# Optimization experiments

Hardware: AMD Instinct MI355X
Metric: run time of the kernel (lower is better)

The kernel has to match this reference:

```python
import jax, jax.numpy as jnp
import numpy as np

D_MODEL = 1024
NUM_HEADS = 16
D_K = D_MODEL // NUM_HEADS
B, S = 4, 2048
NEG = -1e20


def setup_inputs() -> dict:
    key = jax.random.key(0)
    ks = jax.random.split(key, 12)
    def lin(kw, kb):
        # torch nn.Linear init: U(-1/sqrt(in), 1/sqrt(in)), weight shape [out, in]
        bound = 1.0 / np.sqrt(D_MODEL)
        W = jax.random.uniform(kw, (D_MODEL, D_MODEL), jnp.float32, -bound, bound)
        b = jax.random.uniform(kb, (D_MODEL,), jnp.float32, -bound, bound)
        return W, b
    Wq, bq = lin(ks[0], ks[1])
    Wk, bk = lin(ks[2], ks[3])
    Wv, bv = lin(ks[4], ks[5])
    Wo, bo = lin(ks[6], ks[7])
    q = jax.random.normal(ks[8], (B, S, D_MODEL), jnp.float32)
    k = jax.random.normal(ks[9], (B, S, D_MODEL), jnp.float32)
    v = jax.random.normal(ks[10], (B, S, D_MODEL), jnp.float32)
    # causal mask, broadcastable [1,1,S,S]; mask==0 positions are masked out
    mask = jnp.tril(jnp.ones((S, S), jnp.int32))[None, None]
    return {"q": q, "k": k, "v": v, "mask": mask,
            "Wq": Wq, "bq": bq, "Wk": Wk, "bk": bk,
            "Wv": Wv, "bv": bv, "Wo": Wo, "bo": bo}


def _split_heads(x):
    b, s, _ = x.shape
    return x.reshape(b, s, NUM_HEADS, D_K).transpose(0, 2, 1, 3)  # [b,h,s,dk]


def reference(q, k, v, mask, Wq, bq, Wk, bk, Wv, bv, Wo, bo):
    qh = _split_heads(q @ Wq.T + bq)
    kh = _split_heads(k @ Wk.T + bk)
    vh = _split_heads(v @ Wv.T + bv)
    scores = jnp.einsum('bhqd,bhkd->bhqk', qh, kh) / jnp.sqrt(jnp.float32(D_K))
    scores = jnp.where(mask == 0, jnp.float32(NEG), scores)
    attn = jax.nn.softmax(scores, axis=-1)  # dropout is identity in eval mode
    out = jnp.einsum('bhqk,bhkd->bhqd', attn, vh)
    out = out.transpose(0, 2, 1, 3).reshape(q.shape[0], -1, D_MODEL)
    return out @ Wo.T + bo, attn
```

## Files before the change

### kernel.cpp

```cpp
#include <hip/hip_runtime.h>
#include <stdint.h>

#define S_LEN 2048
#define NHEADS 16
#define DK 64
#define DMODEL 1024
#define PS_STRIDE 72
#define S_MASK -3.0e4f

typedef __bf16 bf16;
typedef __bf16 bf16x8 __attribute__((ext_vector_type(8)));
typedef float f32x4 __attribute__((ext_vector_type(4)));
typedef uint32_t u32;

#define MFMA(a, b, c) __builtin_amdgcn_mfma_f32_16x16x32_bf16((a), (b), (c), 0, 0, 0)

__device__ __forceinline__ bf16x8 cvt8(f32x4 a, f32x4 b) {
  bf16x8 w;
  w[0] = (bf16)a[0]; w[1] = (bf16)a[1]; w[2] = (bf16)a[2]; w[3] = (bf16)a[3];
  w[4] = (bf16)b[0]; w[5] = (bf16)b[1]; w[6] = (bf16)b[2]; w[7] = (bf16)b[3];
  return w;
}

__device__ __forceinline__ void async16(const void* g, void* lds_uniform) {
  __builtin_amdgcn_global_load_lds((const __attribute__((address_space(1))) u32*)g,
                                   (__attribute__((address_space(3))) u32*)lds_uniform,
                                   16, 0, 0);
}

__device__ __forceinline__ void stage_tile(const bf16* gbase, size_t rstride,
                                           bf16* buf, int wave, int lane) {
#pragma unroll
  for (int i = 0; i < 2; ++i) {
    int c = i * 256 + wave * 64 + lane;
    int r = c >> 3, ch = c & 7;
    int chg = ch ^ (r & 7);
    const bf16* src = gbase + (size_t)r * rstride + chg * 8;
    char* dst = (char*)buf + (size_t)(i * 256 + wave * 64) * 16;
    async16(src, dst);
  }
}

__global__ __launch_bounds__(256) void cvt_f32_bf16(const float* __restrict__ src,
                                                    bf16* __restrict__ dst, int n8) {
  int stride = gridDim.x * blockDim.x;
  for (int i = blockIdx.x * blockDim.x + threadIdx.x; i < n8; i += stride) {
    f32x4 a = ((const f32x4*)src)[2 * i];
    f32x4 b = ((const f32x4*)src)[2 * i + 1];
    ((bf16x8*)dst)[i] = cvt8(a, b);
  }
}

template <int MODE, typename OutT>
__global__ __launch_bounds__(256, 2) void gemm_bias(const bf16* __restrict__ X,
                                                    const bf16* __restrict__ W,
                                                    const float* __restrict__ bias,
                                                    OutT* __restrict__ out) {
  __shared__ __attribute__((aligned(16))) bf16 At[128 * 32];
  __shared__ __attribute__((aligned(16))) bf16 Bt[128 * 32];
  const int tid = threadIdx.x;
  const int wave = tid >> 6;
  const int lane = tid & 63;
  const int col16 = lane & 15;
  const int kg = lane >> 4;
  const int m0 = blockIdx.x * 128;
  const int n0 = blockIdx.y * 128;
  const int wm = (wave >> 1) * 64;
  const int wn = (wave & 1) * 64;

  f32x4 acc[4][4] = {};

  for (int k0 = 0; k0 < 1024; k0 += 32) {
    __syncthreads();
#pragma unroll
    for (int is = 0; is < 2; ++is) {
      int idx = wave * 64 + is * 256 + lane;
      int row = idx >> 2, ch = idx & 3;
      const char* ga = (const char*)(X + (size_t)(m0 + row) * 1024 + k0) + ch * 16;
      const char* gb = (const char*)(W + (size_t)(n0 + row) * 1024 + k0) + ch * 16;
      async16(ga, (char*)At + (size_t)(wave * 64 + is * 256) * 16);
      async16(gb, (char*)Bt + (size_t)(wave * 64 + is * 256) * 16);
    }
    __syncthreads();

    bf16x8 af[4], bfr[4];
#pragma unroll
    for (int i = 0; i < 4; ++i)
      af[i] = *(const bf16x8*)&At[(wm + i * 16 + col16) * 32 + kg * 8];
#pragma unroll
    for (int j = 0; j < 4; ++j)
      bfr[j] = *(const bf16x8*)&Bt[(wn + j * 16 + col16) * 32 + kg * 8];
#pragma unroll
    for (int i = 0; i < 4; ++i)
#pragma unroll
      for (int j = 0; j < 4; ++j) acc[i][j] = MFMA(af[i], bfr[j], acc[i][j]);
  }

#pragma unroll
  for (int j = 0; j < 4; ++j) {
    int n = n0 + wn + j * 16 + col16;
    float bj = bias[n];
#pragma unroll
    for (int i = 0; i < 4; ++i) {
#pragma unroll
      for (int r = 0; r < 4; ++r) {
        int m = m0 + wm + i * 16 + kg * 4 + r;
        float v = acc[i][j][r] + bj;
        size_t o;
        if (MODE == 0) {
          o = (size_t)m * 1024 + n;
        } else {
          int b = m >> 11, s = m & 2047;
          int h = n >> 6, d = n & 63;
          if (MODE == 1)
            o = ((size_t)(b * 16 + h) * 2048 + s) * 64 + d;
          else
            o = ((size_t)(b * 16 + h) * 64 + d) * 2048 + s;
        }
        out[o] = (OutT)v;
      }
    }
  }
}

__global__ __launch_bounds__(256, 2) void attn_fused(const bf16* __restrict__ Qh,
                                                     const bf16* __restrict__ Kh,
                                                     const bf16* __restrict__ Vt,
                                                     float* __restrict__ attn,
                                                     bf16* __restrict__ O) {
  __shared__ __attribute__((aligned(16))) bf16 Klds[2][64 * 64];
  __shared__ __attribute__((aligned(16))) bf16 Vlds[2][64 * 64];
  __shared__ __attribute__((aligned(16))) bf16 Ps[128 * PS_STRIDE];
  const int tid = threadIdx.x;
  const int wave = tid >> 6;
  const int lane = tid & 63;
  const int col16 = lane & 15;
  const int kg = lane >> 4;
  const int pr = blockIdx.x;
  const int bh = blockIdx.z * NHEADS + blockIdx.y;

  const bf16* qb = Qh + (size_t)bh * S_LEN * DK;
  const bf16* kb = Kh + (size_t)bh * S_LEN * DK;
  const bf16* vb = Vt + (size_t)bh * DK * S_LEN;
  float* ab = attn + (size_t)bh * S_LEN * S_LEN;
  const int b_ = bh >> 4, h_ = bh & 15;

#pragma unroll 1
  for (int sp = 0; sp < 2; ++sp) {
    const int bq = sp ? (15 - pr) : pr;
    const int q0 = bq * 128;
    const int jt_max = 2 * bq + 1;

    bf16x8 qf[2][2];
#pragma unroll
    for (int fr = 0; fr < 2; ++fr)
#pragma unroll
      for (int kk = 0; kk < 2; ++kk) {
        bf16x8 v = *(const bf16x8*)&qb[(size_t)(q0 + wave * 32 + fr * 16 + col16) * DK +
                                       kk * 32 + kg * 8];
        bf16x8 sc;
#pragma unroll
        for (int e = 0; e < 8; ++e) sc[e] = (bf16)((float)v[e] * 0.125f);
        qf[fr][kk] = sc;
      }

    float l_run[2][4] = {};

    stage_tile(kb, DK, Klds[0], wave, lane);
    __syncthreads();
    int cur = 0;
    for (int jt = 0; jt <= jt_max; ++jt) {
      if (jt < jt_max) stage_tile(kb + (size_t)(jt + 1) * 64 * DK, DK, Klds[cur ^ 1], wave, lane);
      const int j0 = jt * 64;
      f32x4 s[2][4] = {};
#pragma unroll
      for (int kk = 0; kk < 2; ++kk) {
        bf16x8 kf[4];
#pragma unroll
        for (int fc = 0; fc < 4; ++fc) {
          int rr = fc * 16 + col16;
          kf[fc] = *(const bf16x8*)&Klds[cur][rr * 64 + (((kk << 2) + kg) ^ (rr & 7)) * 8];
        }
#pragma unroll
        for (int fr = 0; fr < 2; ++fr)
#pragma unroll
          for (int fc = 0; fc < 4; ++fc) s[fr][fc] = MFMA(qf[fr][kk], kf[fc], s[fr][fc]);
      }
      if (jt >= 2 * bq) {
#pragma unroll
        for (int fr = 0; fr < 2; ++fr)
#pragma unroll
          for (int fc = 0; fc < 4; ++fc)
#pragma unroll
            for (int r = 0; r < 4; ++r) {
              int qi = q0 + wave * 32 + fr * 16 + kg * 4 + r;
              int j = j0 + fc * 16 + col16;
              if (j > qi) s[fr][fc][r] = S_MASK;
            }
      }
#pragma unroll
      for (int fr = 0; fr < 2; ++fr)
#pragma unroll
        for (int r = 0; r < 4; ++r)
          l_run[fr][r] += (__expf(s[fr][0][r]) + __expf(s[fr][1][r])) +
                          (__expf(s[fr][2][r]) + __expf(s[fr][3][r]));
      __syncthreads();
      cur ^= 1;
    }
    float linv[2][4];
#pragma unroll
    for (int fr = 0; fr < 2; ++fr)
#pragma unroll
      for (int r = 0; r < 4; ++r) {
        float l = l_run[fr][r];
#pragma unroll
        for (int dd = 1; dd < 16; dd <<= 1) l += __shfl_xor(l, dd, 64);
        linv[fr][r] = 1.f / l;
      }

    f32x4 o[2][4] = {};
    stage_tile(kb, DK, Klds[0], wave, lane);
    stage_tile(vb, S_LEN, Vlds[0], wave, lane);
    __syncthreads();
    cur = 0;
    for (int jt = 0; jt <= jt_max; ++jt) {
      if (jt < jt_max) {
        stage_tile(kb + (size_t)(jt + 1) * 64 * DK, DK, Klds[cur ^ 1], wave, lane);
        stage_tile(vb + (jt + 1) * 64, S_LEN, Vlds[cur ^ 1], wave, lane);
      }
      const int j0 = jt * 64;
      f32x4 s[2][4] = {};
#pragma unroll
      for (int kk = 0; kk < 2; ++kk) {
        bf16x8 kf[4];
#pragma unroll
        for (int fc = 0; fc < 4; ++fc) {
          int rr = fc * 16 + col16;
          kf[fc] = *(const bf16x8*)&Klds[cur][rr * 64 + (((kk << 2) + kg) ^ (rr & 7)) * 8];
        }
#pragma unroll
        for (int fr = 0; fr < 2; ++fr)
#pragma unroll
          for (int fc = 0; fc < 4; ++fc) s[fr][fc] = MFMA(qf[fr][kk], kf[fc], s[fr][fc]);
      }
      if (jt >= 2 * bq) {
#pragma unroll
        for (int fr = 0; fr < 2; ++fr)
#pragma unroll
          for (int fc = 0; fc < 4; ++fc)
#pragma unroll
            for (int r = 0; r < 4; ++r) {
              int qi = q0 + wave * 32 + fr * 16 + kg * 4 + r;
              int j = j0 + fc * 16 + col16;
              if (j > qi) s[fr][fc][r] = S_MASK;
            }
      }
#pragma unroll
      for (int fr = 0; fr < 2; ++fr)
#pragma unroll
        for (int fc = 0; fc < 4; ++fc)
#pragma unroll
          for (int r = 0; r < 4; ++r) {
            float p = __expf(s[fr][fc][r]) * linv[fr][r];
            int row = wave * 32 + fr * 16 + kg * 4 + r;
            int col = fc * 16 + col16;
            ab[(size_t)(q0 + row) * S_LEN + j0 + col] = p;
            Ps[row * PS_STRIDE + col] = (bf16)p;
          }
      __syncthreads();
#pragma unroll
      for (int kk = 0; kk < 2; ++kk) {
        bf16x8 pf[2], vf[4];
#pragma unroll
        for (int fr = 0; fr < 2; ++fr)
          pf[fr] = *(const bf16x8*)&Ps[(wave * 32 + fr * 16 + col16) * PS_STRIDE + kk * 32 + kg * 8];
#pragma unroll
        for (int fc = 0; fc < 4; ++fc) {
          int rr = fc * 16 + col16;
          vf[fc] = *(const bf16x8*)&Vlds[cur][rr * 64 + (((kk << 2) + kg) ^ (rr & 7)) * 8];
        }
#pragma unroll
        for (int fr = 0; fr < 2; ++fr)
#pragma unroll
          for (int fc = 0; fc < 4; ++fc) o[fr][fc] = MFMA(pf[fr], vf[fc], o[fr][fc]);
      }
      __syncthreads();
      cur ^= 1;
    }

    {
      f32x4 z = {0.f, 0.f, 0.f, 0.f};
      for (int jt = jt_max + 1; jt < S_LEN / 64; ++jt) {
        const int j0 = jt * 64;
#pragma unroll
        for (int rep = 0; rep < 8; ++rep) {
          int idx = rep * 256 + tid;
          int row = idx >> 4, c = idx & 15;
          *(f32x4*)&ab[(size_t)(q0 + row) * S_LEN + j0 + c * 4] = z;
        }
      }
    }

#pragma unroll
    for (int fr = 0; fr < 2; ++fr)
#pragma unroll
      for (int fc = 0; fc < 4; ++fc)
#pragma unroll
        for (int r = 0; r < 4; ++r) {
          size_t row = (size_t)b_ * S_LEN + q0 + wave * 32 + fr * 16 + kg * 4 + r;
          O[row * DMODEL + h_ * 64 + fc * 16 + col16] = (bf16)o[fr][fc][r];
        }
  }
}

static inline void cvt_launch(const float* src, bf16* dst, size_t n, hipStream_t stream) {
  int n8 = (int)(n / 8);
  int blocks = (n8 + 255) / 256;
  if (blocks > 2048) blocks = 2048;
  cvt_f32_bf16<<<blocks, 256, 0, stream>>>(src, dst, n8);
}

extern "C" void kernel_launch(void* const* d_in, const int* in_sizes, int n_in,
                              void* d_out, int out_size, void* d_ws, size_t ws_size,
                              hipStream_t stream) {
  (void)in_sizes; (void)n_in; (void)out_size; (void)ws_size;
  const float* q = (const float*)d_in[0];
  const float* k = (const float*)d_in[1];
  const float* v = (const float*)d_in[2];
  const float* Wq = (const float*)d_in[4];
  const float* bq = (const float*)d_in[5];
  const float* Wk = (const float*)d_in[6];
  const float* bk = (const float*)d_in[7];
  const float* Wv = (const float*)d_in[8];
  const float* bv = (const float*)d_in[9];
  const float* Wo = (const float*)d_in[10];
  const float* bo = (const float*)d_in[11];

  float* out = (float*)d_out;
  float* attn = out + (size_t)8192 * 1024;

  const size_t NX = (size_t)8192 * 1024;
  const size_t NW = (size_t)1024 * 1024;
  bf16* Qh = (bf16*)d_ws;
  bf16* Kh = Qh + NX;
  bf16* Vt = Kh + NX;
  bf16* O = Vt + NX;
  bf16* Xbf = O + NX;
  bf16* Wbf = Xbf + NX;

  dim3 gg(64, 8), bb(256);

  cvt_launch(q, Xbf, NX, stream);
  cvt_launch(Wq, Wbf, NW, stream);
  gemm_bias<1, bf16><<<gg, bb, 0, stream>>>(Xbf, Wbf, bq, Qh);

  cvt_launch(k, Xbf, NX, stream);
  cvt_launch(Wk, Wbf, NW, stream);
  gemm_bias<1, bf16><<<gg, bb, 0, stream>>>(Xbf, Wbf, bk, Kh);

  cvt_launch(v, Xbf, NX, stream);
  cvt_launch(Wv, Wbf, NW, stream);
  gemm_bias<2, bf16><<<gg, bb, 0, stream>>>(Xbf, Wbf, bv, Vt);

  attn_fused<<<dim3(8, NHEADS, 4), bb, 0, stream>>>(Qh, Kh, Vt, attn, O);

  cvt_launch(Wo, Wbf, NW, stream);
  gemm_bias<0, float><<<gg, bb, 0, stream>>>(O, Wbf, bo, out);
}
```

Baseline: 529.4 us.

## Use eight waves per attention block with one 16-row fragment each

```diff
diff --git a/kernel.cpp b/kernel.cpp
--- a/kernel.cpp
+++ b/kernel.cpp
@@ -28,17 +28,14 @@
                                    16, 0, 0);
 }
 
-__device__ __forceinline__ void stage_tile(const bf16* gbase, size_t rstride,
-                                           bf16* buf, int wave, int lane) {
-#pragma unroll
-  for (int i = 0; i < 2; ++i) {
-    int c = i * 256 + wave * 64 + lane;
-    int r = c >> 3, ch = c & 7;
-    int chg = ch ^ (r & 7);
-    const bf16* src = gbase + (size_t)r * rstride + chg * 8;
-    char* dst = (char*)buf + (size_t)(i * 256 + wave * 64) * 16;
-    async16(src, dst);
-  }
+__device__ __forceinline__ void stage_tile8(const bf16* gbase, size_t rstride,
+                                            bf16* buf, int wave, int lane) {
+  int c = wave * 64 + lane;
+  int r = c >> 3, ch = c & 7;
+  int chg = ch ^ (r & 7);
+  const bf16* src = gbase + (size_t)r * rstride + chg * 8;
+  char* dst = (char*)buf + (size_t)(wave * 64) * 16;
+  async16(src, dst);
 }
 
 __global__ __launch_bounds__(256) void cvt_f32_bf16(const float* __restrict__ src,
@@ -123,7 +120,7 @@
   }
 }
 
-__global__ __launch_bounds__(256, 2) void attn_fused(const bf16* __restrict__ Qh,
+__global__ __launch_bounds__(512, 4) void attn_fused(const bf16* __restrict__ Qh,
                                                      const bf16* __restrict__ Kh,
                                                      const bf16* __restrict__ Vt,
                                                      float* __restrict__ attn,
@@ -151,28 +148,25 @@
     const int q0 = bq * 128;
     const int jt_max = 2 * bq + 1;
 
-    bf16x8 qf[2][2];
-#pragma unroll
-    for (int fr = 0; fr < 2; ++fr)
-#pragma unroll
-      for (int kk = 0; kk < 2; ++kk) {
-        bf16x8 v = *(const bf16x8*)&qb[(size_t)(q0 + wave * 32 + fr * 16 + col16) * DK +
-                                       kk * 32 + kg * 8];
-        bf16x8 sc;
-#pragma unroll
-        for (int e = 0; e < 8; ++e) sc[e] = (bf16)((float)v[e] * 0.125f);
-        qf[fr][kk] = sc;
-      }
-
-    float l_run[2][4] = {};
-
-    stage_tile(kb, DK, Klds[0], wave, lane);
+    bf16x8 qf[2];
+#pragma unroll
+    for (int kk = 0; kk < 2; ++kk) {
+      bf16x8 v = *(const bf16x8*)&qb[(size_t)(q0 + wave * 16 + col16) * DK + kk * 32 + kg * 8];
+      bf16x8 sc;
+#pragma unroll
+      for (int e = 0; e < 8; ++e) sc[e] = (bf16)((float)v[e] * 0.125f);
+      qf[kk] = sc;
+    }
+
+    float l_run[4] = {};
+
+    stage_tile8(kb, DK, Klds[0], wave, lane);
     __syncthreads();
     int cur = 0;
     for (int jt = 0; jt <= jt_max; ++jt) {
-      if (jt < jt_max) stage_tile(kb + (size_t)(jt + 1) * 64 * DK, DK, Klds[cur ^ 1], wave, lane);
+      if (jt < jt_max) stage_tile8(kb + (size_t)(jt + 1) * 64 * DK, DK, Klds[cur ^ 1], wave, lane);
       const int j0 = jt * 64;
-      f32x4 s[2][4] = {};
+      f32x4 s[4] = {};
 #pragma unroll
       for (int kk = 0; kk < 2; ++kk) {
         bf16x8 kf[4];
@@ -182,54 +176,45 @@
           kf[fc] = *(const bf16x8*)&Klds[cur][rr * 64 + (((kk << 2) + kg) ^ (rr & 7)) * 8];
         }
 #pragma unroll
-        for (int fr = 0; fr < 2; ++fr)
-#pragma unroll
-          for (int fc = 0; fc < 4; ++fc) s[fr][fc] = MFMA(qf[fr][kk], kf[fc], s[fr][fc]);
+        for (int fc = 0; fc < 4; ++fc) s[fc] = MFMA(qf[kk], kf[fc], s[fc]);
       }
       if (jt >= 2 * bq) {
 #pragma unroll
-        for (int fr = 0; fr < 2; ++fr)
-#pragma unroll
-          for (int fc = 0; fc < 4; ++fc)
-#pragma unroll
-            for (int r = 0; r < 4; ++r) {
-              int qi = q0 + wave * 32 + fr * 16 + kg * 4 + r;
-              int j = j0 + fc * 16 + col16;
-              if (j > qi) s[fr][fc][r] = S_MASK;
-            }
-      }
-#pragma unroll
-      for (int fr = 0; fr < 2; ++fr)
-#pragma unroll
-        for (int r = 0; r < 4; ++r)
-          l_run[fr][r] += (__expf(s[fr][0][r]) + __expf(s[fr][1][r])) +
-                          (__expf(s[fr][2][r]) + __expf(s[fr][3][r]));
+        for (int fc = 0; fc < 4; ++fc)
+#pragma unroll
+          for (int r = 0; r < 4; ++r) {
+            int qi = q0 + wave * 16 + kg * 4 + r;
+            int j = j0 + fc * 16 + col16;
+            if (j > qi) s[fc][r] = S_MASK;
+          }
+      }
+#pragma unroll
+      for (int r = 0; r < 4; ++r)
+        l_run[r] += (__expf(s[0][r]) + __expf(s[1][r])) + (__expf(s[2][r]) + __expf(s[3][r]));
       __syncthreads();
       cur ^= 1;
     }
-    float linv[2][4];
-#pragma unroll
-    for (int fr = 0; fr < 2; ++fr)
-#pragma unroll
-      for (int r = 0; r < 4; ++r) {
-        float l = l_run[fr][r];
-#pragma unroll
-        for (int dd = 1; dd < 16; dd <<= 1) l += __shfl_xor(l, dd, 64);
-        linv[fr][r] = 1.f / l;
-      }
-
-    f32x4 o[2][4] = {};
-    stage_tile(kb, DK, Klds[0], wave, lane);
-    stage_tile(vb, S_LEN, Vlds[0], wave, lane);
+    float linv[4];
+#pragma unroll
+    for (int r = 0; r < 4; ++r) {
+      float l = l_run[r];
+#pragma unroll
+      for (int dd = 1; dd < 16; dd <<= 1) l += __shfl_xor(l, dd, 64);
+      linv[r] = 1.f / l;
+    }
+
+    f32x4 o[4] = {};
+    stage_tile8(kb, DK, Klds[0], wave, lane);
+    stage_tile8(vb, S_LEN, Vlds[0], wave, lane);
     __syncthreads();
     cur = 0;
     for (int jt = 0; jt <= jt_max; ++jt) {
       if (jt < jt_max) {
-        stage_tile(kb + (size_t)(jt + 1) * 64 * DK, DK, Klds[cur ^ 1], wave, lane);
-        stage_tile(vb + (jt + 1) * 64, S_LEN, Vlds[cur ^ 1], wave, lane);
+        stage_tile8(kb + (size_t)(jt + 1) * 64 * DK, DK, Klds[cur ^ 1], wave, lane);
+        stage_tile8(vb + (jt + 1) * 64, S_LEN, Vlds[cur ^ 1], wave, lane);
       }
       const int j0 = jt * 64;
-      f32x4 s[2][4] = {};
+      f32x4 s[4] = {};
 #pragma unroll
       for (int kk = 0; kk < 2; ++kk) {
         bf16x8 kf[4];
@@ -239,50 +224,40 @@
           kf[fc] = *(const bf16x8*)&Klds[cur][rr * 64 + (((kk << 2) + kg) ^ (rr & 7)) * 8];
         }
 #pragma unroll
-        for (int fr = 0; fr < 2; ++fr)
-#pragma unroll
-          for (int fc = 0; fc < 4; ++fc) s[fr][fc] = MFMA(qf[fr][kk], kf[fc], s[fr][fc]);
+        for (int fc = 0; fc < 4; ++fc) s[fc] = MFMA(qf[kk], kf[fc], s[fc]);
       }
       if (jt >= 2 * bq) {
 #pragma unroll
-        for (int fr = 0; fr < 2; ++fr)
-#pragma unroll
-          for (int fc = 0; fc < 4; ++fc)
-#pragma unroll
-            for (int r = 0; r < 4; ++r) {
-              int qi = q0 + wave * 32 + fr * 16 + kg * 4 + r;
-              int j = j0 + fc * 16 + col16;
-              if (j > qi) s[fr][fc][r] = S_MASK;
-            }
-      }
-#pragma unroll
-      for (int fr = 0; fr < 2; ++fr)
-#pragma unroll
         for (int fc = 0; fc < 4; ++fc)
 #pragma unroll
           for (int r = 0; r < 4; ++r) {
-            float p = __expf(s[fr][fc][r]) * linv[fr][r];
-            int row = wave * 32 + fr * 16 + kg * 4 + r;
-            int col = fc * 16 + col16;
-            ab[(size_t)(q0 + row) * S_LEN + j0 + col] = p;
-            Ps[row * PS_STRIDE + col] = (bf16)p;
+            int qi = q0 + wave * 16 + kg * 4 + r;
+            int j = j0 + fc * 16 + col16;
+            if (j > qi) s[fc][r] = S_MASK;
           }
+      }
+#pragma unroll
+      for (int fc = 0; fc < 4; ++fc)
+#pragma unroll
+        for (int r = 0; r < 4; ++r) {
+          float p = __expf(s[fc][r]) * linv[r];
+          int row = wave * 16 + kg * 4 + r;
+          int col = fc * 16 + col16;
+          ab[(size_t)(q0 + row) * S_LEN + j0 + col] = p;
+          Ps[row * PS_STRIDE + col] = (bf16)p;
+        }
       __syncthreads();
 #pragma unroll
       for (int kk = 0; kk < 2; ++kk) {
-        bf16x8 pf[2], vf[4];
-#pragma unroll
-        for (int fr = 0; fr < 2; ++fr)
-          pf[fr] = *(const bf16x8*)&Ps[(wave * 32 + fr * 16 + col16) * PS_STRIDE + kk * 32 + kg * 8];
+        bf16x8 pf, vf[4];
+        pf = *(const bf16x8*)&Ps[(wave * 16 + col16) * PS_STRIDE + kk * 32 + kg * 8];
 #pragma unroll
         for (int fc = 0; fc < 4; ++fc) {
           int rr = fc * 16 + col16;
           vf[fc] = *(const bf16x8*)&Vlds[cur][rr * 64 + (((kk << 2) + kg) ^ (rr & 7)) * 8];
         }
 #pragma unroll
-        for (int fr = 0; fr < 2; ++fr)
-#pragma unroll
-          for (int fc = 0; fc < 4; ++fc) o[fr][fc] = MFMA(pf[fr], vf[fc], o[fr][fc]);
+        for (int fc = 0; fc < 4; ++fc) o[fc] = MFMA(pf, vf[fc], o[fc]);
       }
       __syncthreads();
       cur ^= 1;
@@ -293,8 +268,8 @@
       for (int jt = jt_max + 1; jt < S_LEN / 64; ++jt) {
         const int j0 = jt * 64;
 #pragma unroll
-        for (int rep = 0; rep < 8; ++rep) {
-          int idx = rep * 256 + tid;
+        for (int rep = 0; rep < 4; ++rep) {
+          int idx = rep * 512 + tid;
           int row = idx >> 4, c = idx & 15;
           *(f32x4*)&ab[(size_t)(q0 + row) * S_LEN + j0 + c * 4] = z;
         }
@@ -302,14 +277,12 @@
     }
 
 #pragma unroll
-    for (int fr = 0; fr < 2; ++fr)
-#pragma unroll
-      for (int fc = 0; fc < 4; ++fc)
-#pragma unroll
-        for (int r = 0; r < 4; ++r) {
-          size_t row = (size_t)b_ * S_LEN + q0 + wave * 32 + fr * 16 + kg * 4 + r;
-          O[row * DMODEL + h_ * 64 + fc * 16 + col16] = (bf16)o[fr][fc][r];
-        }
+    for (int fc = 0; fc < 4; ++fc)
+#pragma unroll
+      for (int r = 0; r < 4; ++r) {
+        size_t row = (size_t)b_ * S_LEN + q0 + wave * 16 + kg * 4 + r;
+        O[row * DMODEL + h_ * 64 + fc * 16 + col16] = (bf16)o[fc][r];
+      }
   }
 }
 
@@ -362,7 +335,7 @@
   cvt_launch(Wv, Wbf, NW, stream);
   gemm_bias<2, bf16><<<gg, bb, 0, stream>>>(Xbf, Wbf, bv, Vt);
 
-  attn_fused<<<dim3(8, NHEADS, 4), bb, 0, stream>>>(Qh, Kh, Vt, attn, O);
+  attn_fused<<<dim3(8, NHEADS, 4), 512, 0, stream>>>(Qh, Kh, Vt, attn, O);
 
   cvt_launch(Wo, Wbf, NW, stream);
   gemm_bias<0, float><<<gg, bb, 0, stream>>>(O, Wbf, bo, out);
```

Result: faster. 491.1 us (-7.2%).
